# Performance work log

Measured on AMD Instinct MI355X. Metric: run time of the kernel, lower is better.

Reference implementation:

```python
import jax, jax.numpy as jnp
import numpy as np

N_FREQS = 6  # PositionEmbedding N_freqs when embedding=='pe'

def _pe(x):
    freqs = (2.0 ** jnp.arange(N_FREQS)).astype(x.dtype)
    fx = x * freqs  # [B,Q,N_FREQS]
    sc = jnp.stack([jnp.sin(fx), jnp.cos(fx)], axis=-1).reshape(fx.shape[0], fx.shape[1], 2 * N_FREQS)
    return jnp.concatenate([x, sc], axis=-1)

def _mlp(h, W1, b1, W2, b2, W3, b3):
    h = jax.nn.relu(h @ W1 + b1)
    h = jax.nn.relu(h @ W2 + b2)
    return h @ W3 + b3

def setup_inputs() -> dict:
    key = jax.random.key(0)
    B, Q, N, D, H = 4, 65536, 8192, 16, 128
    ks = jax.random.split(key, 6)
    coord = jax.random.uniform(ks[0], (B, Q, 1), minval=-1.0, maxval=1.0, dtype=jnp.float32)
    latent = jax.random.normal(ks[1], (B, N, D), dtype=jnp.float32)
    in_dim = (1 + 2 * N_FREQS) + 3 * D  # pe(rel_coord) ++ unfolded feat = 13 + 48 = 61
    def init(k, shp, fan):
        return (jax.random.normal(k, shp, dtype=jnp.float32) / np.float32(np.sqrt(fan)))
    W1 = init(ks[2], (in_dim, H), in_dim); b1 = jnp.zeros((H,), jnp.float32)
    W2 = init(ks[3], (H, H), H);          b2 = jnp.zeros((H,), jnp.float32)
    W3 = init(ks[4], (H, 1), H);          b3 = jnp.zeros((1,), jnp.float32)
    return dict(coord=coord, latent=latent, W1=W1, b1=b1, W2=W2, b2=b2, W3=W3, b3=b3)

def reference(coord, latent, W1, b1, W2, b2, W3, b3):
    B, Q, _ = coord.shape
    N = latent.shape[1]
    # feat_unfold: concat shifted-prev / self / shifted-next along feature dim -> [B,N,3D]
    prev = jnp.concatenate([latent[:, :1], latent[:, :-1]], axis=1)
    nxt = jnp.concatenate([latent[:, 1:], latent[:, -1:]], axis=1)
    feat = jnp.concatenate([prev, latent, nxt], axis=-1)
    # make_coord grid: cell centers in [-1,1]
    grid = (-1.0 + (2.0 * jnp.arange(N, dtype=coord.dtype) + 1.0) / N)
    rx = 1.0 / N           # 2/num_latents/2
    eps_shift = 1e-6
    preds, areas = [], []
    for vx in (-2.0, 0.0):  # eval path vx_lst
        c = jnp.clip(coord + vx * rx + eps_shift, -1.0 + 1e-6, 1.0 - 1e-6)
        idx = jnp.clip(jnp.searchsorted(grid, c[..., 0]), 0, N - 1)  # [B,Q]
        q_coord = grid[idx][..., None]                               # [B,Q,1]
        q_feat = jnp.take_along_axis(feat, idx[..., None], axis=1)   # [B,Q,3D]
        rel = (coord - q_coord) * N                                  # scaled rel coord
        area = jnp.abs(rel[..., 0]) + 1e-9                           # [B,Q]
        inp = jnp.concatenate([_pe(rel), q_feat], axis=-1)           # [B,Q,61]
        preds.append(_mlp(inp, W1, b1, W2, b2, W3, b3))              # [B,Q,1]
        areas.append(area)
    tot = areas[0] + areas[1]
    # local_ensemble: swap areas before weighting
    ret = preds[0] * (areas[1] / tot)[..., None] + preds[1] * (areas[0] / tot)[..., None]
    return ret
```

## Files before the change

### kernel.cpp

```cpp
#include <hip/hip_runtime.h>
#include <hip/hip_bf16.h>

typedef short s8v __attribute__((ext_vector_type(8)));
typedef float f4v __attribute__((ext_vector_type(4)));
typedef unsigned u4v __attribute__((ext_vector_type(4)));

__device__ __forceinline__ unsigned short f2bf(float x) {
  unsigned u = __builtin_bit_cast(unsigned, x);
  u += 0x7fffu + ((u >> 16) & 1u);
  return (unsigned short)(u >> 16);
}
#if __has_builtin(__builtin_amdgcn_cvt_pk_bf16_f32)
__device__ __forceinline__ unsigned pk2(float a, float b) {
  return __builtin_bit_cast(unsigned, __builtin_amdgcn_cvt_pk_bf16_f32(a, b));
}
#else
__device__ __forceinline__ unsigned pk2(float a, float b) {
  unsigned ua = __builtin_bit_cast(unsigned, a) + 0x8000u;
  unsigned ub = __builtin_bit_cast(unsigned, b) + 0x8000u;
  return __builtin_amdgcn_perm(ub, ua, 0x07060302u);
}
#endif

__device__ __forceinline__ void g2lds16(const void* g, void* l) {
  __builtin_amdgcn_global_load_lds(
      (const __attribute__((address_space(1))) unsigned*)g,
      (__attribute__((address_space(3))) unsigned*)l, 16, 0, 0);
}

__global__ void prep_kernel(const float* __restrict__ W1, const float* __restrict__ b1,
                            const float* __restrict__ W2, const float* __restrict__ latent,
                            unsigned short* __restrict__ wsW) {
  int e = blockIdx.x * 256 + threadIdx.x;
  if (e < 8192) {
    int frag = e >> 9, rem = e & 511, lane = rem >> 3, j = rem & 7;
    int h = frag >> 1, ks = frag & 1;
    int q4 = lane >> 4, l15 = lane & 15;
    int k = ks * 32 + q4 * 8 + j;
    int n = h * 16 + l15;
    float v;
    if (k < 13) v = W1[k * 128 + n];
    else if (k == 13) v = b1[n];
    else if (k < 16) v = 0.0f;
    else v = W1[(k - 3) * 128 + n];
    wsW[e] = f2bf(v);
  } else if (e < 24576) {
    int e2 = e - 8192;
    int frag = e2 >> 9, rem = e2 & 511, lane = rem >> 3, j = rem & 7;
    int h2 = frag >> 2, ks = frag & 3;
    int q4 = lane >> 4, l15 = lane & 15;
    int kd = (j < 4) ? (32 * ks + 4 * q4 + j) : (32 * ks + 16 + 4 * q4 + (j - 4));
    int n = h2 * 16 + l15;
    wsW[e] = f2bf(W2[kd * 128 + n]);
  } else {
    int i = e - 24576;
    wsW[e] = f2bf(latent[i]);
  }
}

__global__ __launch_bounds__(256, 2) void lisagon_main(
    const float* __restrict__ coord, const unsigned short* __restrict__ latbf,
    const unsigned short* __restrict__ W1f, const unsigned short* __restrict__ W2f,
    const float* __restrict__ b2, const float* __restrict__ W3,
    const float* __restrict__ b3, float* __restrict__ out) {
  __shared__ __align__(16) unsigned short W2s[16384];
  __shared__ __align__(16) unsigned PE[2][256][4];
  __shared__ __align__(16) float BW[256];

  const int t = threadIdx.x;
  const int lane = t & 63, wv = t >> 6;
  const int l15 = lane & 15, q4 = lane >> 4;

#pragma unroll
  for (int it = 0; it < 8; it++) {
    int off = (it * 4 + wv) * 1024;
    g2lds16((const char*)W2f + off + lane * 16, (char*)W2s + off);
  }
  if (t < 64) {
    ((float4*)BW)[t] = (t < 32) ? ((const float4*)b2)[t] : ((const float4*)W3)[t - 32];
  }
  const s8v* W1fv = (const s8v*)W1f;
  s8v W1r[16];
#pragma unroll
  for (int i = 0; i < 16; i++) W1r[i] = W1fv[i * 64 + lane];

  int idx;
  float area;
  {
    const int Rg = blockIdx.x * 256 + t;
    const int gq = Rg >> 1, p = Rg & 1;
    const float co = coord[gq];
    float c = (co + (p ? 0.0f : -0.000244140625f)) + 1e-6f;
    c = fminf(fmaxf(c, -1.0f + 1e-6f), 1.0f - 1e-6f);
    double u = ((double)c * 8192.0 + 8191.0) * 0.5;
    idx = (int)ceil(u);
    idx = min(max(idx, 0), 8191);
    float qc = ((float)(2 * idx + 1) - 8192.0f) * (1.0f / 8192.0f);
    float rel = (co - qc) * 8192.0f;
    area = fabsf(rel) + 1e-9f;
    float v[16];
    v[0] = rel;
    float f = rel;
#pragma unroll
    for (int i = 0; i < 6; i++) {
      v[1 + 2 * i] = __sinf(f);
      v[2 + 2 * i] = __cosf(f);
      f = f + f;
    }
    v[13] = 1.0f;
    v[14] = 0.0f; v[15] = 0.0f;
    uint4 q0, q1;
    q0.x = pk2(v[0], v[1]);   q0.y = pk2(v[2], v[3]);
    q0.z = pk2(v[4], v[5]);   q0.w = pk2(v[6], v[7]);
    q1.x = pk2(v[8], v[9]);   q1.y = pk2(v[10], v[11]);
    q1.z = pk2(v[12], v[13]); q1.w = pk2(v[14], v[15]);
    ((uint4*)PE[0])[t] = q0;
    ((uint4*)PE[1])[t] = q1;
  }

  const size_t bbase = (size_t)(blockIdx.x >> 9) * (8192 * 16);
  const uint4* latv4 = (const uint4*)(latbf + bbase);
  const int rbase = wv * 64;
  s8v Bf[2][4];
#pragma unroll
  for (int rt = 0; rt < 4; rt++) {
    int srcl = rt * 16 + l15;
    int sidx = __shfl(idx, srcl, 64);
    int rp = max(sidx - 1, 0), rn = min(sidx + 1, 8191);
    int c = q4 & 1;
    uint4 g0 = latv4[rp * 2 + c];
    uint4 g1 = latv4[(q4 < 2 ? sidx : rn) * 2 + c];
    uint4 pe = ((const uint4*)PE[c])[rbase + srcl];
    uint4 b0;
    b0.x = q4 < 2 ? pe.x : g0.x;  b0.y = q4 < 2 ? pe.y : g0.y;
    b0.z = q4 < 2 ? pe.z : g0.z;  b0.w = q4 < 2 ? pe.w : g0.w;
    Bf[0][rt] = __builtin_bit_cast(s8v, b0);
    Bf[1][rt] = __builtin_bit_cast(s8v, g1);
  }

  u4v bbv[4][4];
#pragma unroll
  for (int h = 0; h < 8; h++) {
    f4v a[4];
#pragma unroll
    for (int rt = 0; rt < 4; rt++) a[rt] = (f4v){0.f, 0.f, 0.f, 0.f};
#pragma unroll
    for (int ks = 0; ks < 2; ks++) {
#pragma unroll
      for (int rt = 0; rt < 4; rt++)
        a[rt] = __builtin_amdgcn_mfma_f32_16x16x32_bf16(W1r[h * 2 + ks], Bf[ks][rt],
                                                        a[rt], 0, 0, 0);
    }
#pragma unroll
    for (int rt = 0; rt < 4; rt++) {
      bbv[rt][h >> 1][2 * (h & 1)]     = pk2(fmaxf(a[rt][0], 0.f), fmaxf(a[rt][1], 0.f));
      bbv[rt][h >> 1][2 * (h & 1) + 1] = pk2(fmaxf(a[rt][2], 0.f), fmaxf(a[rt][3], 0.f));
    }
  }

  __syncthreads();

  const s8v* W2sv = (const s8v*)W2s;
  float s[4] = {0.f, 0.f, 0.f, 0.f};
#pragma unroll
  for (int h2 = 0; h2 < 8; h2++) {
    f4v a2[4];
    f4v b2v = ((const f4v*)BW)[h2 * 4 + q4];
#pragma unroll
    for (int rt = 0; rt < 4; rt++) a2[rt] = b2v;
#pragma unroll
    for (int ks = 0; ks < 4; ks++) {
      s8v Af = W2sv[(h2 * 4 + ks) * 64 + lane];
#pragma unroll
      for (int rt = 0; rt < 4; rt++)
        a2[rt] = __builtin_amdgcn_mfma_f32_16x16x32_bf16(
            Af, __builtin_bit_cast(s8v, bbv[rt][ks]), a2[rt], 0, 0, 0);
    }
    float4 w3v = ((const float4*)(BW + 128))[h2 * 4 + q4];
#pragma unroll
    for (int rt = 0; rt < 4; rt++) {
      s[rt] += fmaxf(a2[rt][0], 0.f) * w3v.x;
      s[rt] += fmaxf(a2[rt][1], 0.f) * w3v.y;
      s[rt] += fmaxf(a2[rt][2], 0.f) * w3v.z;
      s[rt] += fmaxf(a2[rt][3], 0.f) * w3v.w;
    }
  }

  const float b3s = b3[0];
#pragma unroll
  for (int rt = 0; rt < 4; rt++) {
    float pred = s[rt];
    pred += __shfl_xor(pred, 16, 64);
    pred += __shfl_xor(pred, 32, 64);
    pred += b3s;
    float other = __shfl_xor(pred, 1, 64);
    float a0 = __shfl(area, rt * 16 + l15, 64);
    float a1 = __shfl(area, rt * 16 + l15 + 1, 64);
    if (q4 == 0 && (l15 & 1) == 0) {
      int row0 = rbase + rt * 16 + l15;
      float tot = a0 + a1;
      out[(blockIdx.x * 256 + row0) >> 1] = pred * (a1 / tot) + other * (a0 / tot);
    }
  }
}

extern "C" void kernel_launch(void* const* d_in, const int* in_sizes, int n_in,
                              void* d_out, int out_size, void* d_ws, size_t ws_size,
                              hipStream_t stream) {
  const float* coord  = (const float*)d_in[0];
  const float* latent = (const float*)d_in[1];
  const float* W1 = (const float*)d_in[2];
  const float* b1 = (const float*)d_in[3];
  const float* W2 = (const float*)d_in[4];
  const float* b2 = (const float*)d_in[5];
  const float* W3 = (const float*)d_in[6];
  const float* b3 = (const float*)d_in[7];
  float* out = (float*)d_out;
  unsigned short* wsW = (unsigned short*)d_ws;

  prep_kernel<<<2144, 256, 0, stream>>>(W1, b1, W2, latent, wsW);
  lisagon_main<<<2048, 256, 0, stream>>>(coord, wsW + 24576, wsW, wsW + 8192,
                                         b2, W3, b3, out);
}
```

Before: 97.24 us.

## Read W2 fragments from global instead of LDS and vectorize latent conversion

The main kernel no longer stages W2, b2 and W3 into shared memory. It reads the W2 MFMA fragments and the bias/W3 vectors straight from global memory (L1/L2 cached), which removes the block-wide barrier and frees about 33 KB of LDS per block, possibly allowing more resident blocks. The prep kernel converts the latent four floats per thread with packed bf16 stores, so it needs far fewer blocks. The trade-off is that each wave now fetches W2 from the cache hierarchy rather than LDS, which may add latency inside the second-layer MFMA loop.

Result: slower. 99.24 us (+2.1%).

```diff
diff --git a/kernel.cpp b/kernel.cpp
--- a/kernel.cpp
+++ b/kernel.cpp
@@ -21,12 +21,6 @@
   return __builtin_amdgcn_perm(ub, ua, 0x07060302u);
 }
 #endif
-
-__device__ __forceinline__ void g2lds16(const void* g, void* l) {
-  __builtin_amdgcn_global_load_lds(
-      (const __attribute__((address_space(1))) unsigned*)g,
-      (__attribute__((address_space(3))) unsigned*)l, 16, 0, 0);
-}
 
 __global__ void prep_kernel(const float* __restrict__ W1, const float* __restrict__ b1,
                             const float* __restrict__ W2, const float* __restrict__ latent,
@@ -54,7 +48,11 @@
     wsW[e] = f2bf(W2[kd * 128 + n]);
   } else {
     int i = e - 24576;
-    wsW[e] = f2bf(latent[i]);
+    float4 v = ((const float4*)latent)[i];
+    uint2 o;
+    o.x = pk2(v.x, v.y);
+    o.y = pk2(v.z, v.w);
+    ((uint2*)(wsW + 24576))[i] = o;
   }
 }
 
@@ -63,22 +61,12 @@
     const unsigned short* __restrict__ W1f, const unsigned short* __restrict__ W2f,
     const float* __restrict__ b2, const float* __restrict__ W3,
     const float* __restrict__ b3, float* __restrict__ out) {
-  __shared__ __align__(16) unsigned short W2s[16384];
   __shared__ __align__(16) unsigned PE[2][256][4];
-  __shared__ __align__(16) float BW[256];
 
   const int t = threadIdx.x;
   const int lane = t & 63, wv = t >> 6;
   const int l15 = lane & 15, q4 = lane >> 4;
 
-#pragma unroll
-  for (int it = 0; it < 8; it++) {
-    int off = (it * 4 + wv) * 1024;
-    g2lds16((const char*)W2f + off + lane * 16, (char*)W2s + off);
-  }
-  if (t < 64) {
-    ((float4*)BW)[t] = (t < 32) ? ((const float4*)b2)[t] : ((const float4*)W3)[t - 32];
-  }
   const s8v* W1fv = (const s8v*)W1f;
   s8v W1r[16];
 #pragma unroll
@@ -158,25 +146,23 @@
     }
   }
 
-  __syncthreads();
-
-  const s8v* W2sv = (const s8v*)W2s;
+  const s8v* W2fv = (const s8v*)W2f;
   float s[4] = {0.f, 0.f, 0.f, 0.f};
 #pragma unroll
   for (int h2 = 0; h2 < 8; h2++) {
     f4v a2[4];
-    f4v b2v = ((const f4v*)BW)[h2 * 4 + q4];
+    f4v b2v = ((const f4v*)b2)[h2 * 4 + q4];
 #pragma unroll
     for (int rt = 0; rt < 4; rt++) a2[rt] = b2v;
 #pragma unroll
     for (int ks = 0; ks < 4; ks++) {
-      s8v Af = W2sv[(h2 * 4 + ks) * 64 + lane];
+      s8v Af = W2fv[(h2 * 4 + ks) * 64 + lane];
 #pragma unroll
       for (int rt = 0; rt < 4; rt++)
         a2[rt] = __builtin_amdgcn_mfma_f32_16x16x32_bf16(
             Af, __builtin_bit_cast(s8v, bbv[rt][ks]), a2[rt], 0, 0, 0);
     }
-    float4 w3v = ((const float4*)(BW + 128))[h2 * 4 + q4];
+    float4 w3v = ((const float4*)W3)[h2 * 4 + q4];
 #pragma unroll
     for (int rt = 0; rt < 4; rt++) {
       s[rt] += fmaxf(a2[rt][0], 0.f) * w3v.x;
@@ -218,7 +204,7 @@
   float* out = (float*)d_out;
   unsigned short* wsW = (unsigned short*)d_ws;
 
-  prep_kernel<<<2144, 256, 0, stream>>>(W1, b1, W2, latent, wsW);
+  prep_kernel<<<608, 256, 0, stream>>>(W1, b1, W2, latent, wsW);
   lisagon_main<<<2048, 256, 0, stream>>>(coord, wsW + 24576, wsW, wsW + 8192,
                                          b2, W3, b3, out);
 }
```
